# Performance work log

Hardware: AMD Instinct MI355X
Metric: run time of the kernel (lower is better)

## Reference

```python
import jax, jax.numpy as jnp
import numpy as np

D_MODEL = 512
N_HEADS = 8
N_KV_HEADS = 2
HEAD_DIM = 64
PITCH_VOCAB = 128


def setup_inputs() -> dict:
    key = jax.random.key(0)
    ks = jax.random.split(key, 6)
    B, T, P = 2, 256, 12
    s = lambda fan_in: 1.0 / np.sqrt(fan_in)
    hidden_states = jax.random.normal(ks[0], (B, T, P, D_MODEL), dtype=jnp.float32)
    Wq = jax.random.normal(ks[1], (D_MODEL, N_HEADS * HEAD_DIM), dtype=jnp.float32) * s(D_MODEL)
    Wk = jax.random.normal(ks[2], (D_MODEL, N_KV_HEADS * HEAD_DIM), dtype=jnp.float32) * s(D_MODEL)
    Wv = jax.random.normal(ks[3], (D_MODEL, N_KV_HEADS * HEAD_DIM), dtype=jnp.float32) * s(D_MODEL)
    Wo = jax.random.normal(ks[4], (N_HEADS * HEAD_DIM, D_MODEL), dtype=jnp.float32) * s(N_HEADS * HEAD_DIM)
    pitch_table = jax.random.normal(ks[5], (PITCH_VOCAB, HEAD_DIM), dtype=jnp.float32)
    return {"hidden_states": hidden_states, "Wq": Wq, "Wk": Wk, "Wv": Wv, "Wo": Wo, "pitch_table": pitch_table}


def reference(hidden_states, Wq, Wk, Wv, Wo, pitch_table):
    B, T, P, C = hidden_states.shape
    H, Hkv, d = N_HEADS, N_KV_HEADS, HEAD_DIM
    rep = H // Hkv

    q = (hidden_states @ Wq).reshape(B, T, P, H, d)
    k = (hidden_states @ Wk).reshape(B, T, P, Hkv, d)
    v = (hidden_states @ Wv).reshape(B, T, P, Hkv, d)

    # GQA repeat_kv: (B,T,P,Hkv,d) -> (B,T,P,H,d)
    k = jnp.repeat(k, rep, axis=3)
    v = jnp.repeat(v, rep, axis=3)

    # additive pitch bias on q and k
    pitch_emb = pitch_table[jnp.arange(P)]  # (P, d)
    bias = pitch_emb[None, None, :, None, :]
    q = q + bias
    k = k + bias

    # flatten (T,P) -> S and move heads forward: (B,H,S,d)
    S = T * P
    q = q.transpose(0, 3, 1, 2, 4).reshape(B, H, S, d)
    k = k.transpose(0, 3, 1, 2, 4).reshape(B, H, S, d)
    v = v.transpose(0, 3, 1, 2, 4).reshape(B, H, S, d)

    scale = 1.0 / jnp.sqrt(jnp.asarray(d, dtype=q.dtype))
    attn = jax.nn.softmax(jnp.einsum('bhqd,bhkd->bhqk', q, k) * scale, axis=-1)
    out = jnp.einsum('bhqk,bhkd->bhqd', attn, v)  # (B,H,S,d)

    out = out.reshape(B, H, T, P, d).transpose(0, 2, 3, 1, 4).reshape(B, T, P, H * d)
    return out @ Wo
```

## Files before the change

kernel.cpp:

```cpp
#include <hip/hip_runtime.h>
#include <hip/hip_fp16.h>

#define B_   2
#define T_   256
#define P_   12
#define C_   512
#define H_   8
#define HKV_ 2
#define D_   64
#define S_   (T_ * P_)
#define M_   (B_ * S_)
#define NQKV 768

typedef _Float16 half8_t __attribute__((ext_vector_type(8)));
typedef _Float16 half4_t __attribute__((ext_vector_type(4)));
typedef _Float16 half2_t __attribute__((ext_vector_type(2)));
typedef float    float4_t __attribute__((ext_vector_type(4)));

#if __has_builtin(__builtin_amdgcn_exp2f)
#define EXP2(x) __builtin_amdgcn_exp2f(x)
#else
#define EXP2(x) __expf((x) * 0.69314718f)
#endif

#define SOFT_SHIFT 20.0f
#define SOFT_CLAMP 35.5f
#define QSCALE (0.125f * 1.44269504f)

__global__ __launch_bounds__(256) void prep_kernel(
    const float* __restrict__ hs,
    const float* __restrict__ Wq, const float* __restrict__ Wk,
    const float* __restrict__ Wv, const float* __restrict__ Wo,
    _Float16* __restrict__ hs16,
    _Float16* __restrict__ wcatT,
    _Float16* __restrict__ woT)
{
    const int blk = blockIdx.x;
    const int tid = threadIdx.x;

    if (blk < 160) {
        __shared__ __attribute__((aligned(16))) _Float16 Ts[64][72];
        int t, K, Ndst;
        const float* src; int srcN, col0; _Float16* dst;
        if (blk < 96) { t = blk; K = 512; Ndst = 768; dst = wcatT;
            int nt = t / 8;
            int kt = t % 8;
            int n0 = nt * 64, k0 = kt * 64;
            if (n0 < 512)      { src = Wq; srcN = 512; col0 = n0; }
            else if (n0 < 640) { src = Wk; srcN = 128; col0 = n0 - 512; }
            else               { src = Wv; srcN = 128; col0 = n0 - 640; }
#pragma unroll
            for (int i = 0; i < 4; ++i) {
                int row = i * 16 + (tid >> 4);
                int cg  = tid & 15;
                float4_t v = *(const float4_t*)(src + (size_t)(k0 + row) * srcN + col0 + cg * 4);
                Ts[cg * 4 + 0][row] = (_Float16)v[0];
                Ts[cg * 4 + 1][row] = (_Float16)v[1];
                Ts[cg * 4 + 2][row] = (_Float16)v[2];
                Ts[cg * 4 + 3][row] = (_Float16)v[3];
            }
            __syncthreads();
#pragma unroll
            for (int i = 0; i < 2; ++i) {
                int seg = i * 256 + tid;
                int row = seg >> 3, s = seg & 7;
                *(half8_t*)(dst + (size_t)(n0 + row) * K + k0 + s * 8) =
                    *(const half8_t*)&Ts[row][s * 8];
            }
        } else { t = blk - 96; K = 512; dst = woT;
            int nt = t / 8, kt = t % 8;
            int n0 = nt * 64, k0 = kt * 64;
#pragma unroll
            for (int i = 0; i < 4; ++i) {
                int row = i * 16 + (tid >> 4);
                int cg  = tid & 15;
                float4_t v = *(const float4_t*)(Wo + (size_t)(k0 + row) * 512 + n0 + cg * 4);
                Ts[cg * 4 + 0][row] = (_Float16)v[0];
                Ts[cg * 4 + 1][row] = (_Float16)v[1];
                Ts[cg * 4 + 2][row] = (_Float16)v[2];
                Ts[cg * 4 + 3][row] = (_Float16)v[3];
            }
            __syncthreads();
#pragma unroll
            for (int i = 0; i < 2; ++i) {
                int seg = i * 256 + tid;
                int row = seg >> 3, s = seg & 7;
                *(half8_t*)(dst + (size_t)(n0 + row) * K + k0 + s * 8) =
                    *(const half8_t*)&Ts[row][s * 8];
            }
        }
    } else {
        int base = (blk - 160) * 4096;
#pragma unroll
        for (int i = 0; i < 16; ++i) {
            int f4 = base + i * 256 + tid;
            float4_t v = *(const float4_t*)(hs + (size_t)f4 * 4);
            half4_t hv;
            hv[0] = (_Float16)v[0]; hv[1] = (_Float16)v[1];
            hv[2] = (_Float16)v[2]; hv[3] = (_Float16)v[3];
            *(half4_t*)(hs16 + (size_t)f4 * 4) = hv;
        }
    }
}

__global__ __launch_bounds__(256) void qkv_kernel(
    const _Float16* __restrict__ A,
    const _Float16* __restrict__ WT,
    const float* __restrict__ pitch,
    _Float16* __restrict__ qb,
    _Float16* __restrict__ kb,
    _Float16* __restrict__ vb)
{
    const int m0   = blockIdx.x * 64;
    const int n0   = blockIdx.y * 64;
    const int tid  = threadIdx.x;
    const int wave = tid >> 6;
    const int lane = tid & 63;
    const int ln   = lane & 15;
    const int quad = lane >> 4;

    __shared__ __attribute__((aligned(16))) _Float16 As[64][72];
    __shared__ __attribute__((aligned(16))) _Float16 Bs[64][72];

    float4_t acc[4];
#pragma unroll
    for (int nt = 0; nt < 4; ++nt) acc[nt] = (float4_t){0.f, 0.f, 0.f, 0.f};

    const int srow = tid >> 3;
    const int ss   = tid & 7;

    half8_t ar[2], br[2];
#pragma unroll
    for (int i = 0; i < 2; ++i) {
        int row = i * 32 + srow;
        ar[i] = *(const half8_t*)&A [(size_t)(m0 + row) * 512 + ss * 8];
        br[i] = *(const half8_t*)&WT[(size_t)(n0 + row) * 512 + ss * 8];
    }

    for (int k0 = 0; k0 < 512; k0 += 64) {
        __syncthreads();
#pragma unroll
        for (int i = 0; i < 2; ++i) {
            int row = i * 32 + srow;
            *(half8_t*)&As[row][ss * 8] = ar[i];
            *(half8_t*)&Bs[row][ss * 8] = br[i];
        }
        __syncthreads();

        if (k0 + 64 < 512) {
#pragma unroll
            for (int i = 0; i < 2; ++i) {
                int row = i * 32 + srow;
                ar[i] = *(const half8_t*)&A [(size_t)(m0 + row) * 512 + k0 + 64 + ss * 8];
                br[i] = *(const half8_t*)&WT[(size_t)(n0 + row) * 512 + k0 + 64 + ss * 8];
            }
        }

#pragma unroll
        for (int ks = 0; ks < 2; ++ks) {
            half8_t afrag = *(const half8_t*)&As[wave * 16 + ln][ks * 32 + quad * 8];
#pragma unroll
            for (int nt = 0; nt < 4; ++nt) {
                half8_t bfrag = *(const half8_t*)&Bs[nt * 16 + ln][ks * 32 + quad * 8];
                acc[nt] = __builtin_amdgcn_mfma_f32_16x16x32_f16(afrag, bfrag, acc[nt], 0, 0, 0);
            }
        }
    }

    const int region = (n0 < 512) ? 0 : (n0 < 640 ? 1 : 2);
#pragma unroll
    for (int nt = 0; nt < 4; ++nt) {
        int n = n0 + nt * 16 + ln;
#pragma unroll
        for (int r = 0; r < 4; ++r) {
            int m = m0 + wave * 16 + quad * 4 + r;
            int b = m / S_;
            int s = m - b * S_;
            int p = s % P_;
            float v = acc[nt][r];
            if (region == 0) {
                int h = n >> 6, dd = n & 63;
                v = (v + pitch[p * 64 + dd]) * QSCALE;
                qb[(((size_t)(b * H_ + h)) * S_ + s) * 64 + dd] = (_Float16)v;
            } else if (region == 1) {
                int nn = n - 512, h = nn >> 6, dd = nn & 63;
                v = v + pitch[p * 64 + dd];
                kb[(((size_t)(b * HKV_ + h)) * S_ + s) * 64 + dd] = (_Float16)v;
            } else {
                int nn = n - 640, h = nn >> 6, dd = nn & 63;
                vb[(((size_t)(b * HKV_ + h)) * 64 + dd) * S_ + s] = (_Float16)v;
            }
        }
    }
}

__global__ __launch_bounds__(256) void attn_kernel(
    const _Float16* __restrict__ qbuf,
    const _Float16* __restrict__ kbuf,
    const _Float16* __restrict__ vtb,
    _Float16* __restrict__ ob)
{
    const int qblk = blockIdx.x;
    const int bh   = blockIdx.y;
    const int b    = bh >> 3;
    const int h    = bh & 7;
    const int hkv  = h >> 2;
    const int tid  = threadIdx.x;
    const int w    = tid >> 6;
    const int lane = tid & 63;
    const int ln   = lane & 15;
    const int quad = lane >> 4;

    const _Float16* Q  = qbuf + ((size_t)(b * H_ + h)) * S_ * 64;
    const _Float16* K  = kbuf + ((size_t)(b * HKV_ + hkv)) * S_ * 64;
    const _Float16* Vt = vtb  + ((size_t)(b * HKV_ + hkv)) * 64 * S_;

    __shared__ __attribute__((aligned(16))) _Float16 Ks[64][80];
    __shared__ __attribute__((aligned(16))) _Float16 VT[64][80];
    __shared__ __attribute__((aligned(16))) _Float16 Ps[4][32][40];

    const int qbase = qblk * 64 + (w & 1) * 32;
    const int kk0   = (w >> 1) * 32;

    half8_t qfrag[2][2];
#pragma unroll
    for (int sub = 0; sub < 2; ++sub)
#pragma unroll
        for (int ks = 0; ks < 2; ++ks)
            qfrag[sub][ks] = *(const half8_t*)&Q[(size_t)(qbase + sub * 16 + ln) * 64 + ks * 32 + quad * 8];

    float4_t o[2][4];
#pragma unroll
    for (int sub = 0; sub < 2; ++sub)
#pragma unroll
        for (int nt = 0; nt < 4; ++nt) o[sub][nt] = (float4_t){0.f, 0.f, 0.f, 0.f};
    float lr[2][4] = {{0.f,0.f,0.f,0.f},{0.f,0.f,0.f,0.f}};

    const int j0 = tid >> 3, s0 = tid & 7;
    const int j1 = j0 + 32;
    const int r0 = ((j0 & 1) << 4) | ((j0 >> 5) << 5) | ((j0 >> 1) & 15);
    const int r1 = ((j1 & 1) << 4) | ((j1 >> 5) << 5) | ((j1 >> 1) & 15);

    half8_t kr0, kr1, vr0, vr1;
    kr0 = *(const half8_t*)&K[(size_t)j0 * 64 + s0 * 8];
    kr1 = *(const half8_t*)&K[(size_t)j1 * 64 + s0 * 8];
    vr0 = *(const half8_t*)&Vt[(size_t)j0 * S_ + s0 * 8];
    vr1 = *(const half8_t*)&Vt[(size_t)j1 * S_ + s0 * 8];

    for (int kt = 0; kt < S_; kt += 64) {
        __syncthreads();
        *(half8_t*)&Ks[r0][s0 * 8] = kr0;
        *(half8_t*)&Ks[r1][s0 * 8] = kr1;
        *(half8_t*)&VT[j0][s0 * 8] = vr0;
        *(half8_t*)&VT[j1][s0 * 8] = vr1;
        __syncthreads();

        if (kt + 64 < S_) {
            kr0 = *(const half8_t*)&K[(size_t)(kt + 64 + j0) * 64 + s0 * 8];
            kr1 = *(const half8_t*)&K[(size_t)(kt + 64 + j1) * 64 + s0 * 8];
            vr0 = *(const half8_t*)&Vt[(size_t)j0 * S_ + kt + 64 + s0 * 8];
            vr1 = *(const half8_t*)&Vt[(size_t)j1 * S_ + kt + 64 + s0 * 8];
        }

        float4_t sf[2][2];
#pragma unroll
        for (int c = 0; c < 2; ++c) {
            sf[c][0] = (float4_t){0.f, 0.f, 0.f, 0.f};
            sf[c][1] = (float4_t){0.f, 0.f, 0.f, 0.f};
#pragma unroll
            for (int ks = 0; ks < 2; ++ks) {
                half8_t kf = *(const half8_t*)&Ks[kk0 + c * 16 + ln][ks * 32 + quad * 8];
                sf[c][0] = __builtin_amdgcn_mfma_f32_16x16x32_f16(qfrag[0][ks], kf, sf[c][0], 0, 0, 0);
                sf[c][1] = __builtin_amdgcn_mfma_f32_16x16x32_f16(qfrag[1][ks], kf, sf[c][1], 0, 0, 0);
            }
        }

#pragma unroll
        for (int sub = 0; sub < 2; ++sub) {
#pragma unroll
            for (int r = 0; r < 4; ++r) {
                float p0 = EXP2(fminf(sf[0][sub][r], SOFT_CLAMP) - SOFT_SHIFT);
                float p1 = EXP2(fminf(sf[1][sub][r], SOFT_CLAMP) - SOFT_SHIFT);
                lr[sub][r] += p0 + p1;
                half2_t w2; w2[0] = (_Float16)p0; w2[1] = (_Float16)p1;
                *(half2_t*)&Ps[w][sub * 16 + quad * 4 + r][2 * ln] = w2;
            }
        }

        half8_t pf0 = *(const half8_t*)&Ps[w][ln][quad * 8];
        half8_t pf1 = *(const half8_t*)&Ps[w][16 + ln][quad * 8];
#pragma unroll
        for (int nt = 0; nt < 4; ++nt) {
            half8_t vf = *(const half8_t*)&VT[nt * 16 + ln][kk0 + quad * 8];
            o[0][nt] = __builtin_amdgcn_mfma_f32_16x16x32_f16(pf0, vf, o[0][nt], 0, 0, 0);
            o[1][nt] = __builtin_amdgcn_mfma_f32_16x16x32_f16(pf1, vf, o[1][nt], 0, 0, 0);
        }
    }

    __syncthreads();
    if (w >= 2) {
        float* od = (w == 2) ? (float*)&Ks[0][0] : (float*)&VT[0][0];
#pragma unroll
        for (int sub = 0; sub < 2; ++sub)
#pragma unroll
            for (int nt = 0; nt < 4; ++nt)
                *(float4_t*)&od[lane * 32 + (sub * 4 + nt) * 4] = o[sub][nt];
        float* ld = (float*)&Ps[0][0][0] + (w - 2) * 512;
#pragma unroll
        for (int sub = 0; sub < 2; ++sub)
#pragma unroll
            for (int r = 0; r < 4; ++r)
                ld[lane * 8 + sub * 4 + r] = lr[sub][r];
    }
    __syncthreads();
    if (w < 2) {
        const float* os = (w == 0) ? (const float*)&Ks[0][0] : (const float*)&VT[0][0];
        const float* ls = (const float*)&Ps[0][0][0] + w * 512;
#pragma unroll
        for (int sub = 0; sub < 2; ++sub) {
#pragma unroll
            for (int r = 0; r < 4; ++r) {
                float l = lr[sub][r] + ls[lane * 8 + sub * 4 + r];
                l += __shfl_xor(l, 1);
                l += __shfl_xor(l, 2);
                l += __shfl_xor(l, 4);
                l += __shfl_xor(l, 8);
                float inv = 1.0f / l;
                int qg = qbase + sub * 16 + quad * 4 + r;
                size_t base = ((size_t)(b * S_ + qg)) * 512 + h * 64;
#pragma unroll
                for (int nt = 0; nt < 4; ++nt) {
                    float vsum = o[sub][nt][r] + os[lane * 32 + (sub * 4 + nt) * 4 + r];
                    ob[base + nt * 16 + ln] = (_Float16)(vsum * inv);
                }
            }
        }
    }
}

__global__ __launch_bounds__(256) void proj_out_kernel(
    const _Float16* __restrict__ A,
    const _Float16* __restrict__ WT,
    float* __restrict__ outp)
{
    const int m0   = blockIdx.x * 64;
    const int n0   = blockIdx.y * 64;
    const int tid  = threadIdx.x;
    const int wave = tid >> 6;
    const int lane = tid & 63;
    const int ln   = lane & 15;
    const int quad = lane >> 4;

    __shared__ __attribute__((aligned(16))) _Float16 As[64][72];
    __shared__ __attribute__((aligned(16))) _Float16 Bs[64][72];

    float4_t acc[4];
#pragma unroll
    for (int nt = 0; nt < 4; ++nt) acc[nt] = (float4_t){0.f, 0.f, 0.f, 0.f};

    const int srow = tid >> 3;
    const int ss   = tid & 7;

    half8_t ar[2], br[2];
#pragma unroll
    for (int i = 0; i < 2; ++i) {
        int row = i * 32 + srow;
        ar[i] = *(const half8_t*)&A [(size_t)(m0 + row) * 512 + ss * 8];
        br[i] = *(const half8_t*)&WT[(size_t)(n0 + row) * 512 + ss * 8];
    }

    for (int k0 = 0; k0 < 512; k0 += 64) {
        __syncthreads();
#pragma unroll
        for (int i = 0; i < 2; ++i) {
            int row = i * 32 + srow;
            *(half8_t*)&As[row][ss * 8] = ar[i];
            *(half8_t*)&Bs[row][ss * 8] = br[i];
        }
        __syncthreads();

        if (k0 + 64 < 512) {
#pragma unroll
            for (int i = 0; i < 2; ++i) {
                int row = i * 32 + srow;
                ar[i] = *(const half8_t*)&A [(size_t)(m0 + row) * 512 + k0 + 64 + ss * 8];
                br[i] = *(const half8_t*)&WT[(size_t)(n0 + row) * 512 + k0 + 64 + ss * 8];
            }
        }

#pragma unroll
        for (int ks = 0; ks < 2; ++ks) {
            half8_t afrag = *(const half8_t*)&As[wave * 16 + ln][ks * 32 + quad * 8];
#pragma unroll
            for (int nt = 0; nt < 4; ++nt) {
                half8_t bfrag = *(const half8_t*)&Bs[nt * 16 + ln][ks * 32 + quad * 8];
                acc[nt] = __builtin_amdgcn_mfma_f32_16x16x32_f16(afrag, bfrag, acc[nt], 0, 0, 0);
            }
        }
    }

#pragma unroll
    for (int nt = 0; nt < 4; ++nt) {
        int n = n0 + nt * 16 + ln;
#pragma unroll
        for (int r = 0; r < 4; ++r) {
            int m = m0 + wave * 16 + quad * 4 + r;
            outp[(size_t)m * 512 + n] = acc[nt][r];
        }
    }
}

extern "C" void kernel_launch(void* const* d_in, const int* in_sizes, int n_in,
                              void* d_out, int out_size, void* d_ws, size_t ws_size,
                              hipStream_t stream) {
    const float* hs    = (const float*)d_in[0];
    const float* Wq    = (const float*)d_in[1];
    const float* Wk    = (const float*)d_in[2];
    const float* Wv    = (const float*)d_in[3];
    const float* Wo    = (const float*)d_in[4];
    const float* pitch = (const float*)d_in[5];
    float* out = (float*)d_out;

    _Float16* hs16  = (_Float16*)d_ws;
    _Float16* o_buf = hs16;
    _Float16* q_buf = hs16 + (size_t)M_ * 512;
    _Float16* k_buf = q_buf + (size_t)B_ * H_ * S_ * 64;
    _Float16* v_buf = k_buf + (size_t)B_ * HKV_ * S_ * 64;
    _Float16* wcatT = v_buf + (size_t)B_ * HKV_ * S_ * 64;
    _Float16* woT   = wcatT + (size_t)NQKV * 512;

    prep_kernel<<<352, 256, 0, stream>>>(hs, Wq, Wk, Wv, Wo, hs16, wcatT, woT);
    qkv_kernel<<<dim3(M_ / 64, NQKV / 64), 256, 0, stream>>>(hs16, wcatT, pitch, q_buf, k_buf, v_buf);
    attn_kernel<<<dim3(S_ / 64, B_ * H_), 256, 0, stream>>>(q_buf, k_buf, v_buf, o_buf);
    proj_out_kernel<<<dim3(M_ / 64, 8), 256, 0, stream>>>(o_buf, woT, out);
}
```

Baseline: 165.6 us.

## Split key range across waves, read K/V fragments directly from global

The attention kernel now gives each wave all 64 queries of the block and a quarter of the key sequence, instead of splitting queries and key columns across waves. K and V fragments are loaded straight from global memory into registers, which removes the shared-memory K/V staging and the per-tile block barriers. Partial outputs and row sums are then merged across the four waves through shared memory at the end. Softmax weights are packed with the cvt_pkrtz builtin, and the prep kernel's duplicated transpose code is merged. The costs are much higher register pressure (64 accumulator floats per lane plus 16 row sums), no prefetching of K/V, and a larger final reduction.

```diff
diff --git a/kernel.cpp b/kernel.cpp
--- a/kernel.cpp
+++ b/kernel.cpp
@@ -23,6 +23,14 @@
 #define EXP2(x) __expf((x) * 0.69314718f)
 #endif
 
+static __device__ inline half2_t pack_h2(float a, float b) {
+#if __has_builtin(__builtin_amdgcn_cvt_pkrtz)
+    return __builtin_bit_cast(half2_t, __builtin_amdgcn_cvt_pkrtz(a, b));
+#else
+    half2_t r; r[0] = (_Float16)a; r[1] = (_Float16)b; return r;
+#endif
+}
+
 #define SOFT_SHIFT 20.0f
 #define SOFT_CLAMP 35.5f
 #define QSCALE (0.125f * 1.44269504f)
@@ -40,54 +48,36 @@
 
     if (blk < 160) {
         __shared__ __attribute__((aligned(16))) _Float16 Ts[64][72];
-        int t, K, Ndst;
-        const float* src; int srcN, col0; _Float16* dst;
-        if (blk < 96) { t = blk; K = 512; Ndst = 768; dst = wcatT;
-            int nt = t / 8;
-            int kt = t % 8;
-            int n0 = nt * 64, k0 = kt * 64;
+        const float* src; int srcN, col0; _Float16* dst; int n0, k0;
+        if (blk < 96) {
+            int nt = blk / 8, kt = blk % 8;
+            n0 = nt * 64; k0 = kt * 64; dst = wcatT;
             if (n0 < 512)      { src = Wq; srcN = 512; col0 = n0; }
             else if (n0 < 640) { src = Wk; srcN = 128; col0 = n0 - 512; }
             else               { src = Wv; srcN = 128; col0 = n0 - 640; }
-#pragma unroll
-            for (int i = 0; i < 4; ++i) {
-                int row = i * 16 + (tid >> 4);
-                int cg  = tid & 15;
-                float4_t v = *(const float4_t*)(src + (size_t)(k0 + row) * srcN + col0 + cg * 4);
-                Ts[cg * 4 + 0][row] = (_Float16)v[0];
-                Ts[cg * 4 + 1][row] = (_Float16)v[1];
-                Ts[cg * 4 + 2][row] = (_Float16)v[2];
-                Ts[cg * 4 + 3][row] = (_Float16)v[3];
-            }
-            __syncthreads();
-#pragma unroll
-            for (int i = 0; i < 2; ++i) {
-                int seg = i * 256 + tid;
-                int row = seg >> 3, s = seg & 7;
-                *(half8_t*)(dst + (size_t)(n0 + row) * K + k0 + s * 8) =
-                    *(const half8_t*)&Ts[row][s * 8];
-            }
-        } else { t = blk - 96; K = 512; dst = woT;
+        } else {
+            int t = blk - 96;
             int nt = t / 8, kt = t % 8;
-            int n0 = nt * 64, k0 = kt * 64;
-#pragma unroll
-            for (int i = 0; i < 4; ++i) {
-                int row = i * 16 + (tid >> 4);
-                int cg  = tid & 15;
-                float4_t v = *(const float4_t*)(Wo + (size_t)(k0 + row) * 512 + n0 + cg * 4);
-                Ts[cg * 4 + 0][row] = (_Float16)v[0];
-                Ts[cg * 4 + 1][row] = (_Float16)v[1];
-                Ts[cg * 4 + 2][row] = (_Float16)v[2];
-                Ts[cg * 4 + 3][row] = (_Float16)v[3];
-            }
-            __syncthreads();
-#pragma unroll
-            for (int i = 0; i < 2; ++i) {
-                int seg = i * 256 + tid;
-                int row = seg >> 3, s = seg & 7;
-                *(half8_t*)(dst + (size_t)(n0 + row) * K + k0 + s * 8) =
-                    *(const half8_t*)&Ts[row][s * 8];
-            }
+            n0 = nt * 64; k0 = kt * 64; dst = woT;
+            src = Wo; srcN = 512; col0 = n0;
+        }
+#pragma unroll
+        for (int i = 0; i < 4; ++i) {
+            int row = i * 16 + (tid >> 4);
+            int cg  = tid & 15;
+            float4_t v = *(const float4_t*)(src + (size_t)(k0 + row) * srcN + col0 + cg * 4);
+            Ts[cg * 4 + 0][row] = (_Float16)v[0];
+            Ts[cg * 4 + 1][row] = (_Float16)v[1];
+            Ts[cg * 4 + 2][row] = (_Float16)v[2];
+            Ts[cg * 4 + 3][row] = (_Float16)v[3];
+        }
+        __syncthreads();
+#pragma unroll
+        for (int i = 0; i < 2; ++i) {
+            int seg = i * 256 + tid;
+            int row = seg >> 3, s = seg & 7;
+            *(half8_t*)(dst + (size_t)(n0 + row) * 512 + k0 + s * 8) =
+                *(const half8_t*)&Ts[row][s * 8];
         }
     } else {
         int base = (blk - 160) * 4096;
@@ -202,7 +192,7 @@
 {
     const int qblk = blockIdx.x;
     const int bh   = blockIdx.y;
-    const int b    = bh >> 3;
+    const int bb   = bh >> 3;
     const int h    = bh & 7;
     const int hkv  = h >> 2;
     const int tid  = threadIdx.x;
@@ -211,128 +201,146 @@
     const int ln   = lane & 15;
     const int quad = lane >> 4;
 
-    const _Float16* Q  = qbuf + ((size_t)(b * H_ + h)) * S_ * 64;
-    const _Float16* K  = kbuf + ((size_t)(b * HKV_ + hkv)) * S_ * 64;
-    const _Float16* Vt = vtb  + ((size_t)(b * HKV_ + hkv)) * 64 * S_;
-
-    __shared__ __attribute__((aligned(16))) _Float16 Ks[64][80];
-    __shared__ __attribute__((aligned(16))) _Float16 VT[64][80];
-    __shared__ __attribute__((aligned(16))) _Float16 Ps[4][32][40];
-
-    const int qbase = qblk * 64 + (w & 1) * 32;
-    const int kk0   = (w >> 1) * 32;
-
-    half8_t qfrag[2][2];
-#pragma unroll
-    for (int sub = 0; sub < 2; ++sub)
+    const _Float16* Q  = qbuf + ((size_t)(bb * H_ + h)) * S_ * 64;
+    const _Float16* K  = kbuf + ((size_t)(bb * HKV_ + hkv)) * S_ * 64;
+    const _Float16* Vt = vtb  + ((size_t)(bb * HKV_ + hkv)) * 64 * S_;
+
+    __shared__ __attribute__((aligned(16))) _Float16 Ps[4][64][72];
+
+    const int q0 = qblk * 64;
+
+    half8_t qf[4][2];
+#pragma unroll
+    for (int sub = 0; sub < 4; ++sub)
 #pragma unroll
         for (int ks = 0; ks < 2; ++ks)
-            qfrag[sub][ks] = *(const half8_t*)&Q[(size_t)(qbase + sub * 16 + ln) * 64 + ks * 32 + quad * 8];
-
-    float4_t o[2][4];
-#pragma unroll
-    for (int sub = 0; sub < 2; ++sub)
+            qf[sub][ks] = *(const half8_t*)&Q[(size_t)(q0 + sub * 16 + ln) * 64 + ks * 32 + quad * 8];
+
+    float4_t o[4][4];
+#pragma unroll
+    for (int sub = 0; sub < 4; ++sub)
 #pragma unroll
         for (int nt = 0; nt < 4; ++nt) o[sub][nt] = (float4_t){0.f, 0.f, 0.f, 0.f};
-    float lr[2][4] = {{0.f,0.f,0.f,0.f},{0.f,0.f,0.f,0.f}};
-
-    const int j0 = tid >> 3, s0 = tid & 7;
-    const int j1 = j0 + 32;
-    const int r0 = ((j0 & 1) << 4) | ((j0 >> 5) << 5) | ((j0 >> 1) & 15);
-    const int r1 = ((j1 & 1) << 4) | ((j1 >> 5) << 5) | ((j1 >> 1) & 15);
-
-    half8_t kr0, kr1, vr0, vr1;
-    kr0 = *(const half8_t*)&K[(size_t)j0 * 64 + s0 * 8];
-    kr1 = *(const half8_t*)&K[(size_t)j1 * 64 + s0 * 8];
-    vr0 = *(const half8_t*)&Vt[(size_t)j0 * S_ + s0 * 8];
-    vr1 = *(const half8_t*)&Vt[(size_t)j1 * S_ + s0 * 8];
-
-    for (int kt = 0; kt < S_; kt += 64) {
-        __syncthreads();
-        *(half8_t*)&Ks[r0][s0 * 8] = kr0;
-        *(half8_t*)&Ks[r1][s0 * 8] = kr1;
-        *(half8_t*)&VT[j0][s0 * 8] = vr0;
-        *(half8_t*)&VT[j1][s0 * 8] = vr1;
-        __syncthreads();
-
-        if (kt + 64 < S_) {
-            kr0 = *(const half8_t*)&K[(size_t)(kt + 64 + j0) * 64 + s0 * 8];
-            kr1 = *(const half8_t*)&K[(size_t)(kt + 64 + j1) * 64 + s0 * 8];
-            vr0 = *(const half8_t*)&Vt[(size_t)j0 * S_ + kt + 64 + s0 * 8];
-            vr1 = *(const half8_t*)&Vt[(size_t)j1 * S_ + kt + 64 + s0 * 8];
-        }
-
-        float4_t sf[2][2];
-#pragma unroll
-        for (int c = 0; c < 2; ++c) {
-            sf[c][0] = (float4_t){0.f, 0.f, 0.f, 0.f};
-            sf[c][1] = (float4_t){0.f, 0.f, 0.f, 0.f};
-#pragma unroll
-            for (int ks = 0; ks < 2; ++ks) {
-                half8_t kf = *(const half8_t*)&Ks[kk0 + c * 16 + ln][ks * 32 + quad * 8];
-                sf[c][0] = __builtin_amdgcn_mfma_f32_16x16x32_f16(qfrag[0][ks], kf, sf[c][0], 0, 0, 0);
-                sf[c][1] = __builtin_amdgcn_mfma_f32_16x16x32_f16(qfrag[1][ks], kf, sf[c][1], 0, 0, 0);
-            }
-        }
-
-#pragma unroll
-        for (int sub = 0; sub < 2; ++sub) {
-#pragma unroll
-            for (int r = 0; r < 4; ++r) {
-                float p0 = EXP2(fminf(sf[0][sub][r], SOFT_CLAMP) - SOFT_SHIFT);
-                float p1 = EXP2(fminf(sf[1][sub][r], SOFT_CLAMP) - SOFT_SHIFT);
-                lr[sub][r] += p0 + p1;
-                half2_t w2; w2[0] = (_Float16)p0; w2[1] = (_Float16)p1;
-                *(half2_t*)&Ps[w][sub * 16 + quad * 4 + r][2 * ln] = w2;
-            }
-        }
-
-        half8_t pf0 = *(const half8_t*)&Ps[w][ln][quad * 8];
-        half8_t pf1 = *(const half8_t*)&Ps[w][16 + ln][quad * 8];
-#pragma unroll
-        for (int nt = 0; nt < 4; ++nt) {
-            half8_t vf = *(const half8_t*)&VT[nt * 16 + ln][kk0 + quad * 8];
-            o[0][nt] = __builtin_amdgcn_mfma_f32_16x16x32_f16(pf0, vf, o[0][nt], 0, 0, 0);
-            o[1][nt] = __builtin_amdgcn_mfma_f32_16x16x32_f16(pf1, vf, o[1][nt], 0, 0, 0);
-        }
-    }
-
+    float lr[16];
+#pragma unroll
+    for (int i = 0; i < 16; ++i) lr[i] = 0.f;
+
+    const int kt0 = w * (S_ / 4);
+
+    for (int it = 0; it < S_ / 4 / 64; ++it) {
+        const int kt = kt0 + it * 64;
+        const _Float16* Kp = K + (size_t)kt * 64;
+
+#pragma unroll
+        for (int cp = 0; cp < 2; ++cp) {
+            half8_t kfa[2][2];
+#pragma unroll
+            for (int i = 0; i < 2; ++i) {
+                const _Float16* kr = Kp + (size_t)(4 * ln + 2 * cp + i) * 64;
+                kfa[i][0] = *(const half8_t*)&kr[quad * 8];
+                kfa[i][1] = *(const half8_t*)&kr[32 + quad * 8];
+            }
+#pragma unroll
+            for (int sub = 0; sub < 4; ++sub) {
+                float4_t s0 = (float4_t){0.f, 0.f, 0.f, 0.f};
+                float4_t s1 = (float4_t){0.f, 0.f, 0.f, 0.f};
+                s0 = __builtin_amdgcn_mfma_f32_16x16x32_f16(qf[sub][0], kfa[0][0], s0, 0, 0, 0);
+                s0 = __builtin_amdgcn_mfma_f32_16x16x32_f16(qf[sub][1], kfa[0][1], s0, 0, 0, 0);
+                s1 = __builtin_amdgcn_mfma_f32_16x16x32_f16(qf[sub][0], kfa[1][0], s1, 0, 0, 0);
+                s1 = __builtin_amdgcn_mfma_f32_16x16x32_f16(qf[sub][1], kfa[1][1], s1, 0, 0, 0);
+#pragma unroll
+                for (int r = 0; r < 4; ++r) {
+                    float p0 = EXP2(fminf(s0[r], SOFT_CLAMP) - SOFT_SHIFT);
+                    float p1 = EXP2(fminf(s1[r], SOFT_CLAMP) - SOFT_SHIFT);
+                    half2_t pk = pack_h2(p0, p1);
+                    lr[sub * 4 + r] += p0 + p1;
+                    *(half2_t*)&Ps[w][sub * 16 + quad * 4 + r][4 * ln + 2 * cp] = pk;
+                }
+            }
+        }
+
+        half8_t vf[4][2];
+#pragma unroll
+        for (int nt = 0; nt < 4; ++nt)
+#pragma unroll
+            for (int pk = 0; pk < 2; ++pk)
+                vf[nt][pk] = *(const half8_t*)&Vt[(size_t)(nt * 16 + ln) * S_ + kt + pk * 32 + quad * 8];
+
+#pragma unroll
+        for (int sub = 0; sub < 4; ++sub) {
+            half8_t pf0 = *(const half8_t*)&Ps[w][sub * 16 + ln][quad * 8];
+            half8_t pf1 = *(const half8_t*)&Ps[w][sub * 16 + ln][32 + quad * 8];
+#pragma unroll
+            for (int nt = 0; nt < 4; ++nt) {
+                o[sub][nt] = __builtin_amdgcn_mfma_f32_16x16x32_f16(pf0, vf[nt][0], o[sub][nt], 0, 0, 0);
+                o[sub][nt] = __builtin_amdgcn_mfma_f32_16x16x32_f16(pf1, vf[nt][1], o[sub][nt], 0, 0, 0);
+            }
+        }
+    }
+
+#pragma unroll
+    for (int i = 0; i < 16; ++i) {
+        float l = lr[i];
+        l += __shfl_xor(l, 1);
+        l += __shfl_xor(l, 2);
+        l += __shfl_xor(l, 4);
+        l += __shfl_xor(l, 8);
+        lr[i] = l;
+    }
+
+    float* bufA = (float*)&Ps[0][0][0];
+    float* bufB = bufA + 65 * 68;
+
+    __syncthreads();
+    if (w < 2) {
+        float* bf = w ? bufB : bufA;
+#pragma unroll
+        for (int sub = 0; sub < 4; ++sub) {
+#pragma unroll
+            for (int nt = 0; nt < 4; ++nt)
+                *(float4_t*)&bf[(nt * 16 + ln) * 68 + sub * 16 + quad * 4] = o[sub][nt];
+            if (ln == 0) {
+                float4_t lv = {lr[sub * 4 + 0], lr[sub * 4 + 1], lr[sub * 4 + 2], lr[sub * 4 + 3]};
+                *(float4_t*)&bf[64 * 68 + sub * 16 + quad * 4] = lv;
+            }
+        }
+    }
     __syncthreads();
     if (w >= 2) {
-        float* od = (w == 2) ? (float*)&Ks[0][0] : (float*)&VT[0][0];
-#pragma unroll
-        for (int sub = 0; sub < 2; ++sub)
-#pragma unroll
-            for (int nt = 0; nt < 4; ++nt)
-                *(float4_t*)&od[lane * 32 + (sub * 4 + nt) * 4] = o[sub][nt];
-        float* ld = (float*)&Ps[0][0][0] + (w - 2) * 512;
-#pragma unroll
-        for (int sub = 0; sub < 2; ++sub)
-#pragma unroll
-            for (int r = 0; r < 4; ++r)
-                ld[lane * 8 + sub * 4 + r] = lr[sub][r];
+        float* bf = (w == 3) ? bufB : bufA;
+#pragma unroll
+        for (int sub = 0; sub < 4; ++sub) {
+#pragma unroll
+            for (int nt = 0; nt < 4; ++nt) {
+                float4_t t = *(const float4_t*)&bf[(nt * 16 + ln) * 68 + sub * 16 + quad * 4];
+                t += o[sub][nt];
+                *(float4_t*)&bf[(nt * 16 + ln) * 68 + sub * 16 + quad * 4] = t;
+            }
+            if (ln == 0) {
+                float4_t t = *(const float4_t*)&bf[64 * 68 + sub * 16 + quad * 4];
+                t[0] += lr[sub * 4 + 0]; t[1] += lr[sub * 4 + 1];
+                t[2] += lr[sub * 4 + 2]; t[3] += lr[sub * 4 + 3];
+                *(float4_t*)&bf[64 * 68 + sub * 16 + quad * 4] = t;
+            }
+        }
     }
     __syncthreads();
-    if (w < 2) {
-        const float* os = (w == 0) ? (const float*)&Ks[0][0] : (const float*)&VT[0][0];
-        const float* ls = (const float*)&Ps[0][0][0] + w * 512;
-#pragma unroll
-        for (int sub = 0; sub < 2; ++sub) {
+    {
+        const int sub = w;
+        float4_t la = *(const float4_t*)&bufA[64 * 68 + sub * 16 + quad * 4];
+        float4_t lb = *(const float4_t*)&bufB[64 * 68 + sub * 16 + quad * 4];
+        float inv[4];
+#pragma unroll
+        for (int r = 0; r < 4; ++r) inv[r] = 1.0f / (la[r] + lb[r]);
+#pragma unroll
+        for (int nt = 0; nt < 4; ++nt) {
+            float4_t av = *(const float4_t*)&bufA[(nt * 16 + ln) * 68 + sub * 16 + quad * 4];
+            float4_t bv = *(const float4_t*)&bufB[(nt * 16 + ln) * 68 + sub * 16 + quad * 4];
 #pragma unroll
             for (int r = 0; r < 4; ++r) {
-                float l = lr[sub][r] + ls[lane * 8 + sub * 4 + r];
-                l += __shfl_xor(l, 1);
-                l += __shfl_xor(l, 2);
-                l += __shfl_xor(l, 4);
-                l += __shfl_xor(l, 8);
-                float inv = 1.0f / l;
-                int qg = qbase + sub * 16 + quad * 4 + r;
-                size_t base = ((size_t)(b * S_ + qg)) * 512 + h * 64;
-#pragma unroll
-                for (int nt = 0; nt < 4; ++nt) {
-                    float vsum = o[sub][nt][r] + os[lane * 32 + (sub * 4 + nt) * 4 + r];
-                    ob[base + nt * 16 + ln] = (_Float16)(vsum * inv);
-                }
+                int qg = q0 + sub * 16 + quad * 4 + r;
+                ob[((size_t)(bb * S_ + qg)) * 512 + h * 64 + nt * 16 + ln] =
+                    (_Float16)((av[r] + bv[r]) * inv[r]);
             }
         }
     }
```

Measured after the change: 180.2 us. 8.8% more time.
